# Kernel optimization log

Hardware: AMD Instinct MI355X
Metric: run time of the kernel (lower is better)

## Reference

```python
import jax, jax.numpy as jnp
import numpy as np

# DenoiseTransform(h=10, template_window_size=7, search_window_size=21)
KS = 7                 # odd template window -> kernel_size (7, 7)
SIGMA_COLOR = 10.0     # float(h)
SIGMA_SPACE = 21.0     # float(search_window_size), same for y and x


def _gauss1d(ks, sigma):
    # kornia.get_gaussian_kernel1d: centered, normalized to sum 1
    x = jnp.arange(ks, dtype=jnp.float32) - ks // 2
    g = jnp.exp(-0.5 * (x / sigma) ** 2)
    return g / g.sum()


def setup_inputs() -> dict:
    key = jax.random.key(0)
    # batch of 8 RGB 512x512 images in [0, 1]
    img = jax.random.uniform(key, (8, 3, 512, 512), dtype=jnp.float32)
    return {"img": img}


def reference(img):
    """kornia.filters.bilateral_blur(img, (7,7), 10.0, (21.0,21.0)),
    border_type='reflect', color_distance_type='l1'.
    Fused over the 7x7 window: never materializes (B,C,H,W,49)."""
    ks = KS
    pad = ks // 2
    space = jnp.outer(_gauss1d(ks, SIGMA_SPACE), _gauss1d(ks, SIGMA_SPACE))  # (ks, ks)
    B, C, H, W = img.shape
    padded = jnp.pad(img, ((0, 0), (0, 0), (pad, pad), (pad, pad)), mode="reflect")
    num = jnp.zeros_like(img)                      # (B, C, H, W)
    den = jnp.zeros((B, 1, H, W), dtype=img.dtype)  # (B, 1, H, W)
    neg_half_inv_sc2 = -0.5 / (SIGMA_COLOR ** 2)
    for i in range(ks):          # fixed small 7x7 window -> static unrolled loop
        for j in range(ks):
            patch = jax.lax.dynamic_slice(padded, (0, 0, i, j), (B, C, H, W))
            # L1 color distance over channels, then squared (kornia default 'l1')
            d = jnp.abs(patch - img).sum(axis=1, keepdims=True)  # (B,1,H,W)
            w = space[i, j] * jnp.exp(neg_half_inv_sc2 * d * d)   # (B,1,H,W)
            num = num + w * patch
            den = den + w
    return num / den
```

## Files before the change

### kernel.cpp

```cpp
#include <hip/hip_runtime.h>

#define BB 8
#define HH 512
#define WW 512
#define HW (HH * WW)

__global__ __launch_bounds__(256) void bilateral_kernel(const float* __restrict__ in,
                                                        float* __restrict__ out) {
    int idx = blockIdx.x * 256 + threadIdx.x;
    int x = idx & (WW - 1);
    int y = (idx >> 9) & (HH - 1);
    int b = idx >> 18;

    const float* p0 = in + (size_t)b * 3 * HW;
    const float* p1 = p0 + HW;
    const float* p2 = p1 + HW;
    int cidx = y * WW + x;

    float c0 = p0[cidx], c1 = p1[cidx], c2 = p2[cidx];

    const float sw[7] = {0.98984784f, 0.99547514f, 0.99886688f, 1.0f,
                         0.99886688f, 0.99547514f, 0.98984784f};

    float num0 = 0.f, num1 = 0.f, num2 = 0.f, den = 0.f;

    #pragma unroll
    for (int dy = 0; dy < 7; ++dy) {
        int my = y + dy - 3;
        my = my < 0 ? -my : my;
        my = my >= HH ? 2 * HH - 2 - my : my;
        int rowbase = my * WW;
        float wy = sw[dy];
        #pragma unroll
        for (int dx = 0; dx < 7; ++dx) {
            int mx = x + dx - 3;
            mx = mx < 0 ? -mx : mx;
            mx = mx >= WW ? 2 * WW - 2 - mx : mx;
            int o = rowbase + mx;
            float q0 = p0[o], q1 = p1[o], q2 = p2[o];
            float d = fabsf(q0 - c0) + fabsf(q1 - c1) + fabsf(q2 - c2);
            float w = wy * sw[dx] * __expf(-0.005f * d * d);
            num0 += w * q0;
            num1 += w * q1;
            num2 += w * q2;
            den  += w;
        }
    }

    float inv = 1.0f / den;
    size_t obase = (size_t)b * 3 * HW + cidx;
    out[obase]          = num0 * inv;
    out[obase + HW]     = num1 * inv;
    out[obase + 2 * HW] = num2 * inv;
}

extern "C" void kernel_launch(void* const* d_in, const int* in_sizes, int n_in,
                              void* d_out, int out_size, void* d_ws, size_t ws_size,
                              hipStream_t stream) {
    const float* in = (const float*)d_in[0];
    float* out = (float*)d_out;
    int total = BB * HH * WW;
    int blocks = total / 256;
    bilateral_kernel<<<blocks, 256, 0, stream>>>(in, out);
}
```

Measured before the change: 51.76 us.

## Stage halo tiles in LDS and compute two pixels per thread

Each 32x16 output tile now cooperatively loads its 3-channel halo region (with reflect padding) into shared memory, and the 7x7 window is read from LDS instead of global memory. Each thread computes two horizontally adjacent pixels, reusing one row of 8 loaded values for both windows, and uses float2 LDS loads and stores. The exp is replaced by a hardware exp2 with a prescaled constant. The aim is to cut redundant global and cache traffic and the per-tap index arithmetic, at the cost of LDS usage, a block-wide sync, and more registers per thread.

```diff
diff --git a/kernel.cpp b/kernel.cpp
--- a/kernel.cpp
+++ b/kernel.cpp
@@ -5,53 +5,99 @@
 #define WW 512
 #define HW (HH * WW)
 
-__global__ __launch_bounds__(256) void bilateral_kernel(const float* __restrict__ in,
-                                                        float* __restrict__ out) {
-    int idx = blockIdx.x * 256 + threadIdx.x;
-    int x = idx & (WW - 1);
-    int y = (idx >> 9) & (HH - 1);
-    int b = idx >> 18;
+#define TW 32
+#define TH 16
+#define LR 22
+#define LC 38
+#define LS 40
 
-    const float* p0 = in + (size_t)b * 3 * HW;
-    const float* p1 = p0 + HW;
-    const float* p2 = p1 + HW;
-    int cidx = y * WW + x;
+__device__ __forceinline__ int reflect512(int v) {
+    v = v < 0 ? -v : v;
+    return v >= 512 ? 1022 - v : v;
+}
 
-    float c0 = p0[cidx], c1 = p1[cidx], c2 = p2[cidx];
+__global__ __launch_bounds__(256) void bilateral_lds(const float* __restrict__ in,
+                                                     float* __restrict__ out) {
+    __shared__ float lds[3 * LR * LS];
 
-    const float sw[7] = {0.98984784f, 0.99547514f, 0.99886688f, 1.0f,
-                         0.99886688f, 0.99547514f, 0.98984784f};
+    const int bx = blockIdx.x & 15;
+    const int by = (blockIdx.x >> 4) & 31;
+    const int b  = blockIdx.x >> 9;
+    const int x0 = bx * TW, y0 = by * TH;
+    const int tid = threadIdx.y * 16 + threadIdx.x;
 
-    float num0 = 0.f, num1 = 0.f, num2 = 0.f, den = 0.f;
+    const float* __restrict__ src = in + (size_t)b * 3 * HW;
+
+    for (int e = tid; e < 3 * LR * LC; e += 256) {
+        int ch  = e / (LR * LC);
+        int rem = e - ch * (LR * LC);
+        int r   = rem / LC;
+        int c   = rem - r * LC;
+        int gy  = reflect512(y0 + r - 3);
+        int gx  = reflect512(x0 + c - 3);
+        lds[ch * (LR * LS) + r * LS + c] = src[ch * HW + gy * WW + gx];
+    }
+    __syncthreads();
+
+    const int tx = threadIdx.x, ty = threadIdx.y;
+    const int wbase = ty * LS + 2 * tx;
+    const float* L0 = lds;
+    const float* L1 = lds + LR * LS;
+    const float* L2 = lds + 2 * LR * LS;
+
+    const float cA0 = L0[wbase + 3 * LS + 3], cB0 = L0[wbase + 3 * LS + 4];
+    const float cA1 = L1[wbase + 3 * LS + 3], cB1 = L1[wbase + 3 * LS + 4];
+    const float cA2 = L2[wbase + 3 * LS + 3], cB2 = L2[wbase + 3 * LS + 4];
+
+    float nA0 = 0.f, nA1 = 0.f, nA2 = 0.f, dnA = 0.f;
+    float nB0 = 0.f, nB1 = 0.f, nB2 = 0.f, dnB = 0.f;
+
+    const float swv[7] = {0.98984784f, 0.99547514f, 0.99886688f, 1.0f,
+                          0.99886688f, 0.99547514f, 0.98984784f};
+    const float K2 = -0.00721347520445f;
 
     #pragma unroll
     for (int dy = 0; dy < 7; ++dy) {
-        int my = y + dy - 3;
-        my = my < 0 ? -my : my;
-        my = my >= HH ? 2 * HH - 2 - my : my;
-        int rowbase = my * WW;
-        float wy = sw[dy];
+        const int ro = wbase + dy * LS;
+        float2 u0 = *(const float2*)(L0 + ro);
+        float2 u1 = *(const float2*)(L0 + ro + 2);
+        float2 u2 = *(const float2*)(L0 + ro + 4);
+        float2 u3 = *(const float2*)(L0 + ro + 6);
+        float2 v0 = *(const float2*)(L1 + ro);
+        float2 v1 = *(const float2*)(L1 + ro + 2);
+        float2 v2 = *(const float2*)(L1 + ro + 4);
+        float2 v3 = *(const float2*)(L1 + ro + 6);
+        float2 w0 = *(const float2*)(L2 + ro);
+        float2 w1 = *(const float2*)(L2 + ro + 2);
+        float2 w2 = *(const float2*)(L2 + ro + 4);
+        float2 w3 = *(const float2*)(L2 + ro + 6);
+
+        float q0[8] = {u0.x, u0.y, u1.x, u1.y, u2.x, u2.y, u3.x, u3.y};
+        float q1[8] = {v0.x, v0.y, v1.x, v1.y, v2.x, v2.y, v3.x, v3.y};
+        float q2[8] = {w0.x, w0.y, w1.x, w1.y, w2.x, w2.y, w3.x, w3.y};
+
+        const float wy = swv[dy];
         #pragma unroll
         for (int dx = 0; dx < 7; ++dx) {
-            int mx = x + dx - 3;
-            mx = mx < 0 ? -mx : mx;
-            mx = mx >= WW ? 2 * WW - 2 - mx : mx;
-            int o = rowbase + mx;
-            float q0 = p0[o], q1 = p1[o], q2 = p2[o];
-            float d = fabsf(q0 - c0) + fabsf(q1 - c1) + fabsf(q2 - c2);
-            float w = wy * sw[dx] * __expf(-0.005f * d * d);
-            num0 += w * q0;
-            num1 += w * q1;
-            num2 += w * q2;
-            den  += w;
+            const float sc = wy * swv[dx];
+            {
+                float d = fabsf(q0[dx] - cA0) + fabsf(q1[dx] - cA1) + fabsf(q2[dx] - cA2);
+                float w = sc * __builtin_amdgcn_exp2f(K2 * (d * d));
+                nA0 += w * q0[dx]; nA1 += w * q1[dx]; nA2 += w * q2[dx]; dnA += w;
+            }
+            {
+                float d = fabsf(q0[dx+1] - cB0) + fabsf(q1[dx+1] - cB1) + fabsf(q2[dx+1] - cB2);
+                float w = sc * __builtin_amdgcn_exp2f(K2 * (d * d));
+                nB0 += w * q0[dx+1]; nB1 += w * q1[dx+1]; nB2 += w * q2[dx+1]; dnB += w;
+            }
         }
     }
 
-    float inv = 1.0f / den;
-    size_t obase = (size_t)b * 3 * HW + cidx;
-    out[obase]          = num0 * inv;
-    out[obase + HW]     = num1 * inv;
-    out[obase + 2 * HW] = num2 * inv;
+    const float iA = 1.0f / dnA, iB = 1.0f / dnB;
+    size_t ob = (size_t)b * 3 * HW + (size_t)(y0 + ty) * WW + x0 + 2 * tx;
+    *(float2*)(out + ob)          = make_float2(nA0 * iA, nB0 * iB);
+    *(float2*)(out + ob + HW)     = make_float2(nA1 * iA, nB1 * iB);
+    *(float2*)(out + ob + 2 * HW) = make_float2(nA2 * iA, nB2 * iB);
 }
 
 extern "C" void kernel_launch(void* const* d_in, const int* in_sizes, int n_in,
@@ -59,7 +105,7 @@
                               hipStream_t stream) {
     const float* in = (const float*)d_in[0];
     float* out = (float*)d_out;
-    int total = BB * HH * WW;
-    int blocks = total / 256;
-    bilateral_kernel<<<blocks, 256, 0, stream>>>(in, out);
+    dim3 block(16, 16, 1);
+    int blocks = (WW / TW) * (HH / TH) * BB;
+    bilateral_lds<<<blocks, block, 0, stream>>>(in, out);
 }
```

Result: no change. 51.72 us (-0.1%).

## March each thread down a 16-row strip with a register-resident 7x7 window

Applied to the files above, without the earlier changes.

Each thread now produces 16 vertically consecutive output pixels. It keeps a rolling 7-row by 7-column window of all three channels in registers and loads only one new row per step, instead of re-reading all 49 neighbours for every pixel. The spatial weight is folded into an exp2 argument as log-domain constants, so each tap needs one fma and one exp2 instead of separate multiplies. The price is heavy register pressure (147 window floats plus 21 prefetch temporaries) and a grid of only 512 blocks, both of which can limit occupancy and risk spills.

```diff
diff --git a/kernel.cpp b/kernel.cpp
--- a/kernel.cpp
+++ b/kernel.cpp
@@ -4,54 +4,88 @@
 #define HH 512
 #define WW 512
 #define HW (HH * WW)
+#define STRIP 16
 
-__global__ __launch_bounds__(256) void bilateral_kernel(const float* __restrict__ in,
-                                                        float* __restrict__ out) {
-    int idx = blockIdx.x * 256 + threadIdx.x;
-    int x = idx & (WW - 1);
-    int y = (idx >> 9) & (HH - 1);
-    int b = idx >> 18;
+__device__ __forceinline__ int reflect512(int v) {
+    v = v < 0 ? -v : v;
+    return v >= 512 ? 1022 - v : v;
+}
 
-    const float* p0 = in + (size_t)b * 3 * HW;
-    const float* p1 = p0 + HW;
-    const float* p2 = p1 + HW;
-    int cidx = y * WW + x;
+__global__ __launch_bounds__(256, 2) void bilateral_march(const float* __restrict__ in,
+                                                          float* __restrict__ out) {
+    const int blk   = blockIdx.x;
+    const int b     = blk >> 6;
+    const int rem   = blk & 63;
+    const int strip = rem >> 1;
+    const int xh    = rem & 1;
+    const int x     = xh * 256 + threadIdx.x;
+    const int ys    = strip * STRIP;
 
-    float c0 = p0[cidx], c1 = p1[cidx], c2 = p2[cidx];
+    const float* __restrict__ p0 = in + (size_t)b * 3 * HW;
+    const float* __restrict__ p1 = p0 + HW;
+    const float* __restrict__ p2 = p1 + HW;
 
-    const float sw[7] = {0.98984784f, 0.99547514f, 0.99886688f, 1.0f,
-                         0.99886688f, 0.99547514f, 0.98984784f};
+    int colo[7];
+    #pragma unroll
+    for (int c = 0; c < 7; ++c) colo[c] = reflect512(x - 3 + c);
 
-    float num0 = 0.f, num1 = 0.f, num2 = 0.f, den = 0.f;
-
+    float w0[7][7], w1[7][7], w2[7][7];
     #pragma unroll
-    for (int dy = 0; dy < 7; ++dy) {
-        int my = y + dy - 3;
-        my = my < 0 ? -my : my;
-        my = my >= HH ? 2 * HH - 2 - my : my;
-        int rowbase = my * WW;
-        float wy = sw[dy];
+    for (int j = 0; j < 7; ++j) {
+        int rb = reflect512(ys - 3 + j) * WW;
         #pragma unroll
-        for (int dx = 0; dx < 7; ++dx) {
-            int mx = x + dx - 3;
-            mx = mx < 0 ? -mx : mx;
-            mx = mx >= WW ? 2 * WW - 2 - mx : mx;
-            int o = rowbase + mx;
-            float q0 = p0[o], q1 = p1[o], q2 = p2[o];
-            float d = fabsf(q0 - c0) + fabsf(q1 - c1) + fabsf(q2 - c2);
-            float w = wy * sw[dx] * __expf(-0.005f * d * d);
-            num0 += w * q0;
-            num1 += w * q1;
-            num2 += w * q2;
-            den  += w;
+        for (int c = 0; c < 7; ++c) {
+            int o = rb + colo[c];
+            w0[j][c] = p0[o]; w1[j][c] = p1[o]; w2[j][c] = p2[o];
         }
     }
 
-    float inv = 1.0f / den;
-    size_t obase = (size_t)b * 3 * HW + cidx;
-    out[obase]          = num0 * inv;
-    out[obase + HW]     = num1 * inv;
-    out[obase + 2 * HW] = num2 * inv;
+    const float ls7[7] = {-0.01472138f, -0.00654284f, -0.00163571f, 0.f,
+                          -0.00163571f, -0.00654284f, -0.01472138f};
+    const float K2 = -0.00721347520445f;
+
+    #pragma unroll
+    for (int k = 0; k < STRIP; ++k) {
+        float t0[7], t1[7], t2[7];
+        if (k < STRIP - 1) {
+            int rb = reflect512(ys + k + 4) * WW;
+            #pragma unroll
+            for (int c = 0; c < 7; ++c) {
+                int o = rb + colo[c];
+                t0[c] = p0[o]; t1[c] = p1[o]; t2[c] = p2[o];
+            }
+        }
+
+        const int cs = (k + 3) % 7;
+        const float c0 = w0[cs][3], c1 = w1[cs][3], c2 = w2[cs][3];
+        float n0 = 0.f, n1 = 0.f, n2 = 0.f, dn = 0.f;
+
+        #pragma unroll
+        for (int j = 0; j < 7; ++j) {
+            const int s = (k + j) % 7;
+            #pragma unroll
+            for (int c = 0; c < 7; ++c) {
+                float a0 = w0[s][c], a1 = w1[s][c], a2 = w2[s][c];
+                float d  = fabsf(a0 - c0) + fabsf(a1 - c1) + fabsf(a2 - c2);
+                float wt = __builtin_amdgcn_exp2f(fmaf(K2, d * d, ls7[j] + ls7[c]));
+                n0 += wt * a0; n1 += wt * a1; n2 += wt * a2; dn += wt;
+            }
+        }
+
+        const float inv = 1.0f / dn;
+        size_t ob = (size_t)b * 3 * HW + (size_t)(ys + k) * WW + x;
+        out[ob]          = n0 * inv;
+        out[ob + HW]     = n1 * inv;
+        out[ob + 2 * HW] = n2 * inv;
+
+        if (k < STRIP - 1) {
+            const int ns = k % 7;
+            #pragma unroll
+            for (int c = 0; c < 7; ++c) {
+                w0[ns][c] = t0[c]; w1[ns][c] = t1[c]; w2[ns][c] = t2[c];
+            }
+        }
+    }
 }
 
 extern "C" void kernel_launch(void* const* d_in, const int* in_sizes, int n_in,
@@ -59,7 +93,6 @@
                               hipStream_t stream) {
     const float* in = (const float*)d_in[0];
     float* out = (float*)d_out;
-    int total = BB * HH * WW;
-    int blocks = total / 256;
-    bilateral_kernel<<<blocks, 256, 0, stream>>>(in, out);
+    int blocks = BB * (WW / 256) * (HH / STRIP);
+    bilateral_march<<<blocks, 256, 0, stream>>>(in, out);
 }
```

New measurement: 46.93 us. 1.1x faster.
